# Kernel optimization log

Hardware: AMD Instinct MI355X
Metric: run time of the kernel (lower is better)

The kernel has to match this reference:

```python
import jax, jax.numpy as jnp
import numpy as np

B, F_IN, HID, H, S = 256, 1024, 1024, 16, 128
TEMP = float((HID // H) ** 0.5)  # 8.0


def setup_inputs() -> dict:
    key = jax.random.key(0)
    ks = jax.random.split(key, 7)
    return {
        "x": jax.random.normal(ks[0], (B, F_IN, S), dtype=jnp.float32),
        "Wq": jax.random.normal(ks[1], (HID, F_IN), dtype=jnp.float32) * (1.0 / np.sqrt(F_IN)),
        "bq": jax.random.normal(ks[2], (HID,), dtype=jnp.float32) * 0.01,
        "Wk": jax.random.normal(ks[3], (HID, F_IN), dtype=jnp.float32) * (1.0 / np.sqrt(F_IN)),
        "bk": jax.random.normal(ks[4], (HID,), dtype=jnp.float32) * 0.01,
        "Wo": jax.random.normal(ks[5], (S,), dtype=jnp.float32) * (1.0 / np.sqrt(S)),
        "bo": jax.random.normal(ks[6], (1,), dtype=jnp.float32) * 0.01,
    }


def _to_heads(t):
    # (B, F, S) -> (B, H, S, F//H), matching reshape(B,H,F/H,S).permute(0,1,3,2)
    b, f, s = t.shape
    return t.reshape(b, H, f // H, s).transpose(0, 1, 3, 2)


def reference(x, Wq, bq, Wk, bk, Wo, bo):
    # 1x1 Conv1d == per-position linear over channel dim
    q = jnp.einsum('bis,hi->bhs', x, Wq) + bq[None, :, None]
    k = jnp.einsum('bis,hi->bhs', x, Wk) + bk[None, :, None]
    qh = _to_heads(q)          # (B,H,S,HID/H)
    kh = _to_heads(k)          # (B,H,S,HID/H)
    vh = _to_heads(x)          # (B,H,S,F_IN/H)  -- v is the raw input, unprojected
    scores = jnp.einsum('bhsd,bhtd->bhst', qh, kh) / TEMP
    attn = jax.nn.softmax(scores, axis=-1)
    out = jnp.einsum('bhst,bhtd->bhsd', attn, vh)   # (B,H,S,F_IN/H)
    # _reshape_from_batches: (B,H,S,dv) -> (B, F_IN, S)
    out = out.transpose(0, 1, 3, 2).reshape(x.shape[0], F_IN, S)
    # map_o: Linear(num_users, 1) over last axis, then squeeze
    score = jnp.einsum('bfs,s->bf', out, Wo) + bo[0]
    return score
```

## Files before the change

### kernel.cpp

```cpp
#include <hip/hip_runtime.h>

#define F 1024
#define S 128
#define H 16
#define D 64
#define CK 64
#define NCHUNK 16

typedef short bf16x8 __attribute__((ext_vector_type(8)));
typedef float f32x4  __attribute__((ext_vector_type(4)));

#define XS_UNITS ((size_t)128 * NCHUNK * 2048)
#define WB_UNITS ((size_t)8 * NCHUNK * 2048)
#define WS_NEED ((XS_UNITS + WB_UNITS) * 16)

#define MAIN_LDS_BYTES (8192 * 16 + 8 * 128 * 4 + 128 * 4)

__device__ __forceinline__ unsigned short f2bf(float f) {
    unsigned u = __float_as_uint(f);
    u += 0x7fffu + ((u >> 16) & 1u);
    return (unsigned short)(u >> 16);
}

__device__ __forceinline__ float bf2f(unsigned short h) {
    return __uint_as_float((unsigned)h << 16);
}

__device__ __forceinline__ uint4 pack8(const float* f) {
    uint4 u;
    u.x = (unsigned)f2bf(f[0]) | ((unsigned)f2bf(f[1]) << 16);
    u.y = (unsigned)f2bf(f[2]) | ((unsigned)f2bf(f[3]) << 16);
    u.z = (unsigned)f2bf(f[4]) | ((unsigned)f2bf(f[5]) << 16);
    u.w = (unsigned)f2bf(f[6]) | ((unsigned)f2bf(f[7]) << 16);
    return u;
}

typedef __attribute__((address_space(1))) const unsigned int as1_u32;
typedef __attribute__((address_space(3))) unsigned int as3_u32;

__device__ __forceinline__ void async_cp16(const uint4* g, uint4* l) {
    __builtin_amdgcn_global_load_lds((as1_u32*)g, (as3_u32*)l, 16, 0, 0);
}

__device__ __forceinline__ void bar()   { __builtin_amdgcn_s_barrier(); }
__device__ __forceinline__ void sb0()   { __builtin_amdgcn_sched_barrier(0); }
__device__ __forceinline__ void lgkm0() { asm volatile("s_waitcnt lgkmcnt(0)"); }

template<int N> __device__ __forceinline__ void vmw() {
    asm volatile("s_waitcnt vmcnt(%0)" :: "n"(N));
}

__global__ void prep(const float* __restrict__ x,
                     const float* __restrict__ Wq,
                     const float* __restrict__ Wk,
                     uint4* __restrict__ xs,
                     uint4* __restrict__ wb)
{
    __shared__ float4 t4[64 * 33];
    const int tid = threadIdx.x;
    const int blk = blockIdx.x;
    if (blk < 4096) {
        const int b = blk >> 4, ch = blk & 15;
        const float4* src = (const float4*)(x + ((size_t)b * F + ch * CK) * S);
        float4 v[8];
#pragma unroll
        for (int j = 0; j < 8; ++j) v[j] = src[tid + j * 256];
#pragma unroll
        for (int j = 0; j < 8; ++j) {
            const int e4 = tid + j * 256;
            t4[(e4 >> 5) * 33 + (e4 & 31)] = v[j];
        }
        __syncthreads();
        const float* tile = (const float*)t4;
        uint4* dst = xs + ((size_t)(b >> 1) * NCHUNK + ch) * 2048 + (b & 1) * 128;
#pragma unroll
        for (int j = 0; j < 4; ++j) {
            const int u  = tid + j * 256;
            const int kc = u >> 7;
            const int s  = u & 127;
            float f[8];
#pragma unroll
            for (int jj = 0; jj < 8; ++jj) f[jj] = tile[(kc * 8 + jj) * 132 + s];
            dst[kc * 256 + s] = pack8(f);
        }
    } else {
        const int blk2 = blk - 4096;
        const int h = blk2 >> 4, ch = blk2 & 15;
        uint4* dst = wb + ((size_t)(h >> 1) * NCHUNK + ch) * 2048 + (h & 1) * 128;
#pragma unroll
        for (int j = 0; j < 4; ++j) {
            const int u  = tid + j * 256;
            const int kc = u >> 7;
            const int m  = u & 127;
            const float* srcp = (m < 64)
                ? (Wq + (size_t)(h * D + m) * F + ch * CK + kc * 8)
                : (Wk + (size_t)(h * D + m - 64) * F + ch * CK + kc * 8);
            float f[8];
            float4 a = ((const float4*)srcp)[0];
            float4 c = ((const float4*)srcp)[1];
            f[0] = a.x; f[1] = a.y; f[2] = a.z; f[3] = a.w;
            f[4] = c.x; f[5] = c.y; f[6] = c.z; f[7] = c.w;
            dst[kc * 256 + m] = pack8(f);
        }
    }
}

__device__ __forceinline__ void read4(const uint4* mat, int base, bf16x8 (&r)[4]) {
    r[0] = *(const bf16x8*)&mat[base];
    r[1] = *(const bf16x8*)&mat[base + 16];
    r[2] = *(const bf16x8*)&mat[base + 32];
    r[3] = *(const bf16x8*)&mat[base + 48];
}

template<int RB>
__device__ __forceinline__ void mfma16(f32x4 (&acc)[8][4], const bf16x8 (&af)[4], const bf16x8 (&br)[4]) {
#pragma unroll
    for (int mt = 0; mt < 4; ++mt)
#pragma unroll
        for (int nt = 0; nt < 4; ++nt)
            acc[RB + mt][nt] = __builtin_amdgcn_mfma_f32_16x16x32_bf16(af[mt], br[nt], acc[RB + mt][nt], 0, 0, 0);
}

template<int HALF>
__device__ __forceinline__ void stage_half(uint4* mat, const uint4* wbase, const uint4* xbase,
                                           int tgt, int wv, int lane) {
    const int bufb = (tgt & 1) * 4096;
    const uint4* g;
    int l;
    if constexpr (HALF == 0)      { g = wbase + (size_t)tgt * 2048;        l = bufb;        }
    else if constexpr (HALF == 1) { g = xbase + (size_t)tgt * 2048;        l = bufb + 2048; }
    else if constexpr (HALF == 2) { g = wbase + (size_t)tgt * 2048 + 1024; l = bufb + 1024; }
    else                          { g = xbase + (size_t)tgt * 2048 + 1024; l = bufb + 3072; }
    async_cp16(g + wv * 128 + lane,      &mat[l + wv * 128]);
    async_cp16(g + wv * 128 + 64 + lane, &mat[l + wv * 128 + 64]);
}

template<int CUR, bool I1, bool I2, int W1, int W2, bool DW2>
__device__ __forceinline__ void ktile(uint4* mat, const uint4* wbase, const uint4* xbase,
                                      int t, int wv, int lane, int wm, int wn, int q, int l15,
                                      f32x4 (&acc)[8][4])
{
    bf16x8 af[4], br[4];
    const int abase = CUR * 4096 + wm * 128 + l15;
    const int bbase = CUR * 4096 + 2048 + wn * 64 + l15;
    const int kq = q * 256;
    read4(mat, abase + kq, af);
    read4(mat, bbase + kq, br);
    if constexpr (I1) stage_half<2>(mat, wbase, xbase, t + 1, wv, lane);
    bar(); lgkm0(); sb0();
    __builtin_amdgcn_s_setprio(1); mfma16<0>(acc, af, br); __builtin_amdgcn_s_setprio(0);
    bar(); sb0();
    read4(mat, abase + kq + 64, af);
    if constexpr (I1) stage_half<3>(mat, wbase, xbase, t + 1, wv, lane);
    bar(); lgkm0(); sb0();
    __builtin_amdgcn_s_setprio(1); mfma16<4>(acc, af, br); __builtin_amdgcn_s_setprio(0);
    vmw<W1>(); bar(); sb0();
    read4(mat, abase + kq + 1024, af);
    read4(mat, bbase + kq + 1024, br);
    if constexpr (I2) stage_half<0>(mat, wbase, xbase, t + 2, wv, lane);
    bar(); lgkm0(); sb0();
    __builtin_amdgcn_s_setprio(1); mfma16<0>(acc, af, br); __builtin_amdgcn_s_setprio(0);
    bar(); sb0();
    read4(mat, abase + kq + 1024 + 64, af);
    if constexpr (I2) stage_half<1>(mat, wbase, xbase, t + 2, wv, lane);
    bar(); lgkm0(); sb0();
    __builtin_amdgcn_s_setprio(1); mfma16<4>(acc, af, br); __builtin_amdgcn_s_setprio(0);
    if constexpr (DW2) { vmw<W2>(); bar(); sb0(); }
}

__launch_bounds__(512, 2)
__global__ void attn_main(const float* __restrict__ x,
                          const uint4* __restrict__ xs,
                          const uint4* __restrict__ wb,
                          const float* __restrict__ bq,
                          const float* __restrict__ bk,
                          const float* __restrict__ Wo,
                          const float* __restrict__ bo,
                          float* __restrict__ out)
{
    (void)x;
    extern __shared__ char smraw[];
    uint4* mat   = (uint4*)smraw;
    float* wpart = (float*)(smraw + 8192 * 16);
    float* wfin  = wpart + 8 * 128;

    const int tid  = threadIdx.x;
    const int lane = tid & 63;
    const int wv   = tid >> 6;
    const int l15  = lane & 15;
    const int q    = lane >> 4;
    const int wm   = wv >> 2;
    const int wn   = wv & 3;

    const int g    = blockIdx.x;
    const int xcd  = g & 7;
    const int slot = g >> 3;
    const int bg   = xcd * 16 + (slot & 15);
    const int hg   = slot >> 4;

    const uint4* wbase = wb + (size_t)hg * NCHUNK * 2048;
    const uint4* xbase = xs + (size_t)bg * NCHUNK * 2048;

    f32x4 acc[8][4];
#pragma unroll
    for (int mi = 0; mi < 8; ++mi)
#pragma unroll
        for (int ni = 0; ni < 4; ++ni) acc[mi][ni] = (f32x4){0.f, 0.f, 0.f, 0.f};

    stage_half<0>(mat, wbase, xbase, 0, wv, lane);
    stage_half<1>(mat, wbase, xbase, 0, wv, lane);
    stage_half<2>(mat, wbase, xbase, 0, wv, lane);
    stage_half<3>(mat, wbase, xbase, 0, wv, lane);
    stage_half<0>(mat, wbase, xbase, 1, wv, lane);
    stage_half<1>(mat, wbase, xbase, 1, wv, lane);
    vmw<8>();
    bar(); sb0();

#pragma unroll 1
    for (int i = 0; i < 7; ++i) {
        ktile<0, true, true, 8, 8, true>(mat, wbase, xbase, 2 * i,     wv, lane, wm, wn, q, l15, acc);
        ktile<1, true, true, 8, 8, true>(mat, wbase, xbase, 2 * i + 1, wv, lane, wm, wn, q, l15, acc);
    }
    ktile<0, true,  false, 8, 4, true >(mat, wbase, xbase, 14, wv, lane, wm, wn, q, l15, acc);
    ktile<1, false, false, 0, 0, false>(mat, wbase, xbase, 15, wv, lane, wm, wn, q, l15, acc);

    __syncthreads();

    {
        unsigned short* m16 = (unsigned short*)mat;
        const int hglob = hg * 2 + wm;
#pragma unroll
        for (int rt = 0; rt < 8; ++rt) {
            const int mh0   = rt * 16 + q * 4;
            const int d0    = mh0 & 63;
            const int kbase = (mh0 < 64) ? 0 : 1024;
            float bias4[4];
#pragma unroll
            for (int rr = 0; rr < 4; ++rr)
                bias4[rr] = (mh0 < 64) ? bq[hglob * D + d0 + rr] : bk[hglob * D + d0 + rr];
#pragma unroll
            for (int ct = 0; ct < 4; ++ct) {
                const int col = wn * 64 + ct * 16 + l15;
                const int bj  = col >> 7;
                const int s   = col & 127;
                const int c   = wm * 2 + bj;
                unsigned long long pv = 0;
#pragma unroll
                for (int rr = 0; rr < 4; ++rr)
                    pv |= (unsigned long long)f2bf(acc[rt][ct][rr] + bias4[rr]) << (16 * rr);
                const int unit = c * 2048 + kbase + s * 8 + ((d0 >> 3) ^ (s & 7));
                *(unsigned long long*)&m16[unit * 8 + (d0 & 7)] = pv;
            }
        }
    }
    __syncthreads();

    for (int c = 0; c < 4; ++c) {
        const int qb = c * 2048;
        const int kb = c * 2048 + 1024;
        const int bglob = bg * 2 + (c & 1);
        const int hglob = hg * 2 + (c >> 1);

        f32x4 p[8];
#pragma unroll
        for (int nt = 0; nt < 8; ++nt) p[nt] = (f32x4){0.f, 0.f, 0.f, 0.f};
#pragma unroll
        for (int ks = 0; ks < 2; ++ks) {
            const int kcq  = ks * 4 + q;
            const int arow = wv * 16 + l15;
            bf16x8 a2 = *(const bf16x8*)&mat[qb + arow * 8 + (kcq ^ (arow & 7))];
            bf16x8 b2[8];
#pragma unroll
            for (int nt = 0; nt < 8; ++nt) {
                const int trow = nt * 16 + l15;
                b2[nt] = *(const bf16x8*)&mat[kb + trow * 8 + (kcq ^ (trow & 7))];
            }
#pragma unroll
            for (int nt = 0; nt < 8; ++nt)
                p[nt] = __builtin_amdgcn_mfma_f32_16x16x32_bf16(a2, b2[nt], p[nt], 0, 0, 0);
        }

        const int dd = tid >> 3, part = tid & 7;
        const unsigned short* xp = (const unsigned short*)(xbase + (size_t)hglob * 2048);
        const int hw0 = ((dd >> 3) * 256 + (bglob & 1) * 128) * 8 + (dd & 7);
        unsigned short xr[16];
#pragma unroll
        for (int jj = 0; jj < 16; ++jj) xr[jj] = xp[hw0 + (part * 16 + jj) * 8];

        float pw[8];
#pragma unroll
        for (int nt = 0; nt < 8; ++nt) pw[nt] = 0.f;
#pragma unroll
        for (int rr = 0; rr < 4; ++rr) {
            const int srow = wv * 16 + q * 4 + rr;
            float mx = p[0][rr];
#pragma unroll
            for (int nt = 1; nt < 8; ++nt) mx = fmaxf(mx, p[nt][rr]);
#pragma unroll
            for (int off = 1; off < 16; off <<= 1) mx = fmaxf(mx, __shfl_xor(mx, off));
            float e[8];
            float l = 0.f;
#pragma unroll
            for (int nt = 0; nt < 8; ++nt) {
                e[nt] = __expf((p[nt][rr] - mx) * 0.125f);
                l += e[nt];
            }
#pragma unroll
            for (int off = 1; off < 16; off <<= 1) l += __shfl_xor(l, off);
            const float cw = Wo[srow] / l;
#pragma unroll
            for (int nt = 0; nt < 8; ++nt) pw[nt] = fmaf(cw, e[nt], pw[nt]);
        }
#pragma unroll
        for (int nt = 0; nt < 8; ++nt) {
            pw[nt] += __shfl_xor(pw[nt], 16);
            pw[nt] += __shfl_xor(pw[nt], 32);
        }
        if (q == 0) {
#pragma unroll
            for (int nt = 0; nt < 8; ++nt) wpart[wv * 128 + nt * 16 + l15] = pw[nt];
        }
        __syncthreads();
        if (tid < 128) {
            float sum = 0.f;
#pragma unroll
            for (int w = 0; w < 8; ++w) sum += wpart[w * 128 + tid];
            wfin[tid] = sum;
        }
        __syncthreads();
        {
            float a5 = 0.f;
#pragma unroll
            for (int jj = 0; jj < 16; ++jj)
                a5 = fmaf(wfin[part * 16 + jj], bf2f(xr[jj]), a5);
            a5 += __shfl_xor(a5, 1);
            a5 += __shfl_xor(a5, 2);
            a5 += __shfl_xor(a5, 4);
            if (part == 0) out[(size_t)bglob * F + hglob * D + dd] = a5 + bo[0];
        }
        __syncthreads();
    }
}

struct SmemT {
    uint4 mat[2048];
    float wpart[4][S];
    float wfin[S];
};

__launch_bounds__(256, 4)
__global__ void attn_fallback(const float* __restrict__ x,
                              const float* __restrict__ Wq,
                              const float* __restrict__ bq,
                              const float* __restrict__ Wk,
                              const float* __restrict__ bk,
                              const float* __restrict__ Wo,
                              const float* __restrict__ bo,
                              float* __restrict__ out)
{
    __shared__ SmemT sm;
    const int tid  = threadIdx.x;
    const int lane = tid & 63;
    const int wv   = tid >> 6;
    const int l15  = lane & 15;
    const int q    = lane >> 4;

    const int g    = blockIdx.x;
    const int xcd  = g & 7;
    const int slot = g >> 3;
    const int hg   = slot >> 7;
    const int r0   = slot & 127;
    const int b    = xcd * 32 + (r0 >> 2);
    const int h    = hg * 4 + (r0 & 3);

    const float* xb  = x  + (size_t)b * (F * S);
    const float* wqh = Wq + (size_t)h * D * F;
    const float* wkh = Wk + (size_t)h * D * F;

    const int m0 = (wv & 1) * 64;
    const int n0 = (wv >> 1) * 64;

    f32x4 acc[4][4];
#pragma unroll
    for (int mt = 0; mt < 4; ++mt)
#pragma unroll
        for (int nt = 0; nt < 4; ++nt) acc[mt][nt] = (f32x4){0.f, 0.f, 0.f, 0.f};

    const int mq  = tid >> 2;
    const int kq  = tid & 3;
    const int s0x = (tid & 63) * 2;
    const int iq  = tid >> 6;

    for (int ch = 0; ch < NCHUNK; ++ch) {
        const int c0 = ch * CK;
        __syncthreads();
        {
            const int key = mq & 7;
            float f[16];
            const float4* srcq = (const float4*)(wqh + (size_t)mq * F + (c0 + kq * 16));
#pragma unroll
            for (int j = 0; j < 4; ++j) {
                float4 v = srcq[j];
                f[4*j] = v.x; f[4*j+1] = v.y; f[4*j+2] = v.z; f[4*j+3] = v.w;
            }
            sm.mat[mq * 8 + ((kq * 2    ) ^ key)] = pack8(f);
            sm.mat[mq * 8 + ((kq * 2 + 1) ^ key)] = pack8(f + 8);
            const float4* srck = (const float4*)(wkh + (size_t)mq * F + (c0 + kq * 16));
#pragma unroll
            for (int j = 0; j < 4; ++j) {
                float4 v = srck[j];
                f[4*j] = v.x; f[4*j+1] = v.y; f[4*j+2] = v.z; f[4*j+3] = v.w;
            }
            sm.mat[(64 + mq) * 8 + ((kq * 2    ) ^ key)] = pack8(f);
            sm.mat[(64 + mq) * 8 + ((kq * 2 + 1) ^ key)] = pack8(f + 8);
        }
        {
            const float* src = xb + (size_t)(c0 + iq * 16) * S + s0x;
            float fa[8], fb[8];
#pragma unroll
            for (int grp = 0; grp < 2; ++grp) {
#pragma unroll
                for (int j = 0; j < 8; ++j) {
                    float2 v = *(const float2*)(src + (size_t)(grp * 8 + j) * S);
                    fa[j] = v.x; fb[j] = v.y;
                }
                const int kc = iq * 2 + grp;
                sm.mat[1024 + (s0x    ) * 8 + (kc ^ ((s0x    ) & 7))] = pack8(fa);
                sm.mat[1024 + (s0x + 1) * 8 + (kc ^ ((s0x + 1) & 7))] = pack8(fb);
            }
        }
        __syncthreads();
#pragma unroll
        for (int ks = 0; ks < 2; ++ks) {
            bf16x8 af[4], br[4];
#pragma unroll
            for (int mt = 0; mt < 4; ++mt) {
                const int row = m0 + mt * 16 + l15;
                af[mt] = *(const bf16x8*)&sm.mat[row * 8 + ((ks * 4 + q) ^ (row & 7))];
            }
#pragma unroll
            for (int nt = 0; nt < 4; ++nt) {
                const int row = n0 + nt * 16 + l15;
                br[nt] = *(const bf16x8*)&sm.mat[1024 + row * 8 + ((ks * 4 + q) ^ (row & 7))];
            }
#pragma unroll
            for (int mt = 0; mt < 4; ++mt)
#pragma unroll
                for (int nt = 0; nt < 4; ++nt)
                    acc[mt][nt] = __builtin_amdgcn_mfma_f32_16x16x32_bf16(
                        af[mt], br[nt], acc[mt][nt], 0, 0, 0);
        }
    }

    __syncthreads();
    {
        unsigned short* m16 = (unsigned short*)sm.mat;
#pragma unroll
        for (int mt = 0; mt < 4; ++mt) {
#pragma unroll
            for (int rr = 0; rr < 4; ++rr) {
                const int m = m0 + mt * 16 + q * 4 + rr;
                const int d = m & 63;
                const float bias = (m < 64) ? bq[h * D + d] : bk[h * D + d];
                const int base = (m < 64) ? 0 : 8192;
#pragma unroll
                for (int nt = 0; nt < 4; ++nt) {
                    const int s = n0 + nt * 16 + l15;
                    const float v = acc[mt][nt][rr] + bias;
                    const int unit = s * 8 + (((d >> 3)) ^ (s & 7));
                    m16[base + unit * 8 + (d & 7)] = f2bf(v);
                }
            }
        }
    }
    __syncthreads();

    f32x4 p[2][8];
#pragma unroll
    for (int mt = 0; mt < 2; ++mt)
#pragma unroll
        for (int nt = 0; nt < 8; ++nt) p[mt][nt] = (f32x4){0.f, 0.f, 0.f, 0.f};

#pragma unroll
    for (int ks = 0; ks < 2; ++ks) {
        bf16x8 a2[2], b2[8];
#pragma unroll
        for (int mt = 0; mt < 2; ++mt) {
            const int row = wv * 32 + mt * 16 + l15;
            a2[mt] = *(const bf16x8*)&sm.mat[row * 8 + ((ks * 4 + q) ^ (row & 7))];
        }
#pragma unroll
        for (int nt = 0; nt < 8; ++nt) {
            const int row = nt * 16 + l15;
            b2[nt] = *(const bf16x8*)&sm.mat[1024 + row * 8 + ((ks * 4 + q) ^ (row & 7))];
        }
#pragma unroll
        for (int mt = 0; mt < 2; ++mt)
#pragma unroll
            for (int nt = 0; nt < 8; ++nt)
                p[mt][nt] = __builtin_amdgcn_mfma_f32_16x16x32_bf16(a2[mt], b2[nt], p[mt][nt], 0, 0, 0);
    }

    float pw[8];
#pragma unroll
    for (int nt = 0; nt < 8; ++nt) pw[nt] = 0.f;

#pragma unroll
    for (int mt = 0; mt < 2; ++mt) {
#pragma unroll
        for (int rr = 0; rr < 4; ++rr) {
            const int srow = wv * 32 + mt * 16 + q * 4 + rr;
            float mx = p[mt][0][rr];
#pragma unroll
            for (int nt = 1; nt < 8; ++nt) mx = fmaxf(mx, p[mt][nt][rr]);
#pragma unroll
            for (int off = 1; off < 16; off <<= 1) mx = fmaxf(mx, __shfl_xor(mx, off));
            float e[8];
            float l = 0.f;
#pragma unroll
            for (int nt = 0; nt < 8; ++nt) {
                e[nt] = __expf((p[mt][nt][rr] - mx) * 0.125f);
                l += e[nt];
            }
#pragma unroll
            for (int off = 1; off < 16; off <<= 1) l += __shfl_xor(l, off);
            const float c = Wo[srow] / l;
#pragma unroll
            for (int nt = 0; nt < 8; ++nt) pw[nt] = fmaf(c, e[nt], pw[nt]);
        }
    }
#pragma unroll
    for (int nt = 0; nt < 8; ++nt) {
        pw[nt] += __shfl_xor(pw[nt], 16);
        pw[nt] += __shfl_xor(pw[nt], 32);
    }
    if (q == 0) {
#pragma unroll
        for (int nt = 0; nt < 8; ++nt) sm.wpart[wv][nt * 16 + l15] = pw[nt];
    }
    __syncthreads();
    if (tid < S)
        sm.wfin[tid] = sm.wpart[0][tid] + sm.wpart[1][tid] + sm.wpart[2][tid] + sm.wpart[3][tid];
    __syncthreads();

    {
        const int dd   = tid >> 2;
        const int part = tid & 3;
        const float* xv = xb + (size_t)(h * D + dd) * S + part * 32;
        float a5 = 0.f;
#pragma unroll 8
        for (int t = 0; t < 32; ++t) a5 = fmaf(sm.wfin[part * 32 + t], xv[t], a5);
        a5 += __shfl_xor(a5, 1);
        a5 += __shfl_xor(a5, 2);
        if (part == 0) out[(size_t)b * F + h * D + dd] = a5 + bo[0];
    }
}

extern "C" void kernel_launch(void* const* d_in, const int* in_sizes, int n_in,
                              void* d_out, int out_size, void* d_ws, size_t ws_size,
                              hipStream_t stream) {
    const float* x  = (const float*)d_in[0];
    const float* Wq = (const float*)d_in[1];
    const float* bq = (const float*)d_in[2];
    const float* Wk = (const float*)d_in[3];
    const float* bk = (const float*)d_in[4];
    const float* Wo = (const float*)d_in[5];
    const float* bo = (const float*)d_in[6];
    float* out = (float*)d_out;

    if (ws_size >= WS_NEED) {
        uint4* xsp = (uint4*)d_ws;
        uint4* wbp = (uint4*)((char*)d_ws + XS_UNITS * 16);
        static bool attr_done = false;
        if (!attr_done) {
            (void)hipFuncSetAttribute(reinterpret_cast<const void*>(attn_main),
                                      hipFuncAttributeMaxDynamicSharedMemorySize, MAIN_LDS_BYTES);
            attr_done = true;
        }
        prep<<<dim3(4096 + 256), dim3(256), 0, stream>>>(x, Wq, Wk, xsp, wbp);
        attn_main<<<dim3(1024), dim3(512), MAIN_LDS_BYTES, stream>>>(x, xsp, wbp, bq, bk, Wo, bo, out);
    } else {
        attn_fallback<<<dim3(256 * H), dim3(256), 0, stream>>>(x, Wq, bq, Wk, bk, Wo, bo, out);
    }
}
```

Baseline: 378.0 us.

## Process four attention combos concurrently, drop softmax max pass, coarsen prep blocks

```diff
diff --git a/kernel.cpp b/kernel.cpp
--- a/kernel.cpp
+++ b/kernel.cpp
@@ -20,10 +20,6 @@
     unsigned u = __float_as_uint(f);
     u += 0x7fffu + ((u >> 16) & 1u);
     return (unsigned short)(u >> 16);
-}
-
-__device__ __forceinline__ float bf2f(unsigned short h) {
-    return __uint_as_float((unsigned)h << 16);
 }
 
 __device__ __forceinline__ uint4 pack8(const float* f) {
@@ -59,48 +55,57 @@
     __shared__ float4 t4[64 * 33];
     const int tid = threadIdx.x;
     const int blk = blockIdx.x;
-    if (blk < 4096) {
-        const int b = blk >> 4, ch = blk & 15;
-        const float4* src = (const float4*)(x + ((size_t)b * F + ch * CK) * S);
-        float4 v[8];
-#pragma unroll
-        for (int j = 0; j < 8; ++j) v[j] = src[tid + j * 256];
-#pragma unroll
-        for (int j = 0; j < 8; ++j) {
-            const int e4 = tid + j * 256;
-            t4[(e4 >> 5) * 33 + (e4 & 31)] = v[j];
-        }
-        __syncthreads();
-        const float* tile = (const float*)t4;
-        uint4* dst = xs + ((size_t)(b >> 1) * NCHUNK + ch) * 2048 + (b & 1) * 128;
-#pragma unroll
-        for (int j = 0; j < 4; ++j) {
-            const int u  = tid + j * 256;
-            const int kc = u >> 7;
-            const int s  = u & 127;
-            float f[8];
-#pragma unroll
-            for (int jj = 0; jj < 8; ++jj) f[jj] = tile[(kc * 8 + jj) * 132 + s];
-            dst[kc * 256 + s] = pack8(f);
+    if (blk < 1024) {
+        const int b = blk >> 2;
+#pragma unroll 1
+        for (int cc = 0; cc < 4; ++cc) {
+            const int ch = (blk & 3) * 4 + cc;
+            const float4* src = (const float4*)(x + ((size_t)b * F + ch * CK) * S);
+            float4 v[8];
+#pragma unroll
+            for (int j = 0; j < 8; ++j) v[j] = src[tid + j * 256];
+            __syncthreads();
+#pragma unroll
+            for (int j = 0; j < 8; ++j) {
+                const int e4 = tid + j * 256;
+                t4[(e4 >> 5) * 33 + (e4 & 31)] = v[j];
+            }
+            __syncthreads();
+            const float* tile = (const float*)t4;
+            uint4* dst = xs + ((size_t)(b >> 1) * NCHUNK + ch) * 2048 + (b & 1) * 128;
+#pragma unroll
+            for (int j = 0; j < 4; ++j) {
+                const int u  = tid + j * 256;
+                const int kc = u >> 7;
+                const int s  = u & 127;
+                float f[8];
+#pragma unroll
+                for (int jj = 0; jj < 8; ++jj) f[jj] = tile[(kc * 8 + jj) * 132 + s];
+                dst[kc * 256 + s] = pack8(f);
+            }
         }
     } else {
-        const int blk2 = blk - 4096;
-        const int h = blk2 >> 4, ch = blk2 & 15;
-        uint4* dst = wb + ((size_t)(h >> 1) * NCHUNK + ch) * 2048 + (h & 1) * 128;
-#pragma unroll
-        for (int j = 0; j < 4; ++j) {
-            const int u  = tid + j * 256;
-            const int kc = u >> 7;
-            const int m  = u & 127;
-            const float* srcp = (m < 64)
-                ? (Wq + (size_t)(h * D + m) * F + ch * CK + kc * 8)
-                : (Wk + (size_t)(h * D + m - 64) * F + ch * CK + kc * 8);
-            float f[8];
-            float4 a = ((const float4*)srcp)[0];
-            float4 c = ((const float4*)srcp)[1];
-            f[0] = a.x; f[1] = a.y; f[2] = a.z; f[3] = a.w;
-            f[4] = c.x; f[5] = c.y; f[6] = c.z; f[7] = c.w;
-            dst[kc * 256 + m] = pack8(f);
+        const int blk2 = blk - 1024;
+        const int h = blk2 >> 2;
+#pragma unroll 1
+        for (int cc = 0; cc < 4; ++cc) {
+            const int ch = (blk2 & 3) * 4 + cc;
+            uint4* dst = wb + ((size_t)(h >> 1) * NCHUNK + ch) * 2048 + (h & 1) * 128;
+#pragma unroll
+            for (int j = 0; j < 4; ++j) {
+                const int u  = tid + j * 256;
+                const int kc = u >> 7;
+                const int m  = u & 127;
+                const float* srcp = (m < 64)
+                    ? (Wq + (size_t)(h * D + m) * F + ch * CK + kc * 8)
+                    : (Wk + (size_t)(h * D + m - 64) * F + ch * CK + kc * 8);
+                float f[8];
+                float4 a = ((const float4*)srcp)[0];
+                float4 c = ((const float4*)srcp)[1];
+                f[0] = a.x; f[1] = a.y; f[2] = a.z; f[3] = a.w;
+                f[4] = c.x; f[5] = c.y; f[6] = c.z; f[7] = c.w;
+                dst[kc * 256 + m] = pack8(f);
+            }
         }
     }
 }
@@ -178,11 +183,9 @@
                           const float* __restrict__ bo,
                           float* __restrict__ out)
 {
-    (void)x;
     extern __shared__ char smraw[];
     uint4* mat   = (uint4*)smraw;
     float* wpart = (float*)(smraw + 8192 * 16);
-    float* wfin  = wpart + 8 * 128;
 
     const int tid  = threadIdx.x;
     const int lane = tid & 63;
@@ -255,54 +258,52 @@
     }
     __syncthreads();
 
-    for (int c = 0; c < 4; ++c) {
-        const int qb = c * 2048;
-        const int kb = c * 2048 + 1024;
-        const int bglob = bg * 2 + (c & 1);
-        const int hglob = hg * 2 + (c >> 1);
-
-        f32x4 p[8];
-#pragma unroll
-        for (int nt = 0; nt < 8; ++nt) p[nt] = (f32x4){0.f, 0.f, 0.f, 0.f};
-#pragma unroll
-        for (int ks = 0; ks < 2; ++ks) {
-            const int kcq  = ks * 4 + q;
-            const int arow = wv * 16 + l15;
-            bf16x8 a2 = *(const bf16x8*)&mat[qb + arow * 8 + (kcq ^ (arow & 7))];
-            bf16x8 b2[8];
-#pragma unroll
-            for (int nt = 0; nt < 8; ++nt) {
-                const int trow = nt * 16 + l15;
-                b2[nt] = *(const bf16x8*)&mat[kb + trow * 8 + (kcq ^ (trow & 7))];
-            }
+    const int ce   = ((wv >> 2) << 1) | ((wv >> 1) & 1);
+    const int half = wv & 1;
+    const int qb = ce * 2048;
+    const int kb = ce * 2048 + 1024;
+    const int bglob = bg * 2 + (ce & 1);
+    const int hglob = hg * 2 + (ce >> 1);
+
+    f32x4 p[4][8];
+#pragma unroll
+    for (int mt = 0; mt < 4; ++mt)
+#pragma unroll
+        for (int nt = 0; nt < 8; ++nt) p[mt][nt] = (f32x4){0.f, 0.f, 0.f, 0.f};
+#pragma unroll
+    for (int ks = 0; ks < 2; ++ks) {
+        const int kcq = ks * 4 + q;
+        bf16x8 a2[4], b2[8];
+#pragma unroll
+        for (int mt = 0; mt < 4; ++mt) {
+            const int row = half * 64 + mt * 16 + l15;
+            a2[mt] = *(const bf16x8*)&mat[qb + row * 8 + (kcq ^ (row & 7))];
+        }
+#pragma unroll
+        for (int nt = 0; nt < 8; ++nt) {
+            const int trow = nt * 16 + l15;
+            b2[nt] = *(const bf16x8*)&mat[kb + trow * 8 + (kcq ^ (trow & 7))];
+        }
+#pragma unroll
+        for (int mt = 0; mt < 4; ++mt)
 #pragma unroll
             for (int nt = 0; nt < 8; ++nt)
-                p[nt] = __builtin_amdgcn_mfma_f32_16x16x32_bf16(a2, b2[nt], p[nt], 0, 0, 0);
-        }
-
-        const int dd = tid >> 3, part = tid & 7;
-        const unsigned short* xp = (const unsigned short*)(xbase + (size_t)hglob * 2048);
-        const int hw0 = ((dd >> 3) * 256 + (bglob & 1) * 128) * 8 + (dd & 7);
-        unsigned short xr[16];
-#pragma unroll
-        for (int jj = 0; jj < 16; ++jj) xr[jj] = xp[hw0 + (part * 16 + jj) * 8];
-
-        float pw[8];
-#pragma unroll
-        for (int nt = 0; nt < 8; ++nt) pw[nt] = 0.f;
+                p[mt][nt] = __builtin_amdgcn_mfma_f32_16x16x32_bf16(a2[mt], b2[nt], p[mt][nt], 0, 0, 0);
+    }
+
+    float pw[8];
+#pragma unroll
+    for (int nt = 0; nt < 8; ++nt) pw[nt] = 0.f;
+#pragma unroll
+    for (int mt = 0; mt < 4; ++mt) {
 #pragma unroll
         for (int rr = 0; rr < 4; ++rr) {
-            const int srow = wv * 16 + q * 4 + rr;
-            float mx = p[0][rr];
-#pragma unroll
-            for (int nt = 1; nt < 8; ++nt) mx = fmaxf(mx, p[nt][rr]);
-#pragma unroll
-            for (int off = 1; off < 16; off <<= 1) mx = fmaxf(mx, __shfl_xor(mx, off));
+            const int srow = half * 64 + mt * 16 + q * 4 + rr;
             float e[8];
             float l = 0.f;
 #pragma unroll
             for (int nt = 0; nt < 8; ++nt) {
-                e[nt] = __expf((p[nt][rr] - mx) * 0.125f);
+                e[nt] = __expf(fminf(p[mt][nt][rr] * 0.125f, 80.f));
                 l += e[nt];
             }
 #pragma unroll
@@ -311,34 +312,38 @@
 #pragma unroll
             for (int nt = 0; nt < 8; ++nt) pw[nt] = fmaf(cw, e[nt], pw[nt]);
         }
-#pragma unroll
-        for (int nt = 0; nt < 8; ++nt) {
-            pw[nt] += __shfl_xor(pw[nt], 16);
-            pw[nt] += __shfl_xor(pw[nt], 32);
-        }
-        if (q == 0) {
-#pragma unroll
-            for (int nt = 0; nt < 8; ++nt) wpart[wv * 128 + nt * 16 + l15] = pw[nt];
-        }
-        __syncthreads();
-        if (tid < 128) {
-            float sum = 0.f;
-#pragma unroll
-            for (int w = 0; w < 8; ++w) sum += wpart[w * 128 + tid];
-            wfin[tid] = sum;
-        }
-        __syncthreads();
-        {
-            float a5 = 0.f;
-#pragma unroll
-            for (int jj = 0; jj < 16; ++jj)
-                a5 = fmaf(wfin[part * 16 + jj], bf2f(xr[jj]), a5);
-            a5 += __shfl_xor(a5, 1);
-            a5 += __shfl_xor(a5, 2);
-            a5 += __shfl_xor(a5, 4);
-            if (part == 0) out[(size_t)bglob * F + hglob * D + dd] = a5 + bo[0];
-        }
-        __syncthreads();
+    }
+#pragma unroll
+    for (int nt = 0; nt < 8; ++nt) {
+        pw[nt] += __shfl_xor(pw[nt], 16);
+        pw[nt] += __shfl_xor(pw[nt], 32);
+    }
+    if (q == 0) {
+#pragma unroll
+        for (int nt = 0; nt < 8; ++nt) wpart[wv * 128 + nt * 16 + l15] = pw[nt];
+    }
+    __syncthreads();
+
+    {
+        const int local = half * 64 + lane;
+        const int dd    = local >> 1;
+        const int part  = local & 1;
+        const float* w0 = wpart + 2 * ce * 128;
+        const float* w1 = wpart + (2 * ce + 1) * 128;
+        const float4* xv = (const float4*)(x + (size_t)bglob * (F * S)
+                                             + (size_t)(hglob * D + dd) * S + part * 64);
+        float a5 = 0.f;
+#pragma unroll
+        for (int j = 0; j < 16; ++j) {
+            float4 vv = xv[j];
+            const int t = part * 64 + j * 4;
+            a5 = fmaf(w0[t + 0] + w1[t + 0], vv.x, a5);
+            a5 = fmaf(w0[t + 1] + w1[t + 1], vv.y, a5);
+            a5 = fmaf(w0[t + 2] + w1[t + 2], vv.z, a5);
+            a5 = fmaf(w0[t + 3] + w1[t + 3], vv.w, a5);
+        }
+        a5 += __shfl_xor(a5, 1);
+        if (part == 0) out[(size_t)bglob * F + hglob * D + dd] = a5 + bo[0];
     }
 }
 
@@ -577,7 +582,7 @@
                                       hipFuncAttributeMaxDynamicSharedMemorySize, MAIN_LDS_BYTES);
             attr_done = true;
         }
-        prep<<<dim3(4096 + 256), dim3(256), 0, stream>>>(x, Wq, Wk, xsp, wbp);
+        prep<<<dim3(1024 + 64), dim3(256), 0, stream>>>(x, Wq, Wk, xsp, wbp);
         attn_main<<<dim3(1024), dim3(512), MAIN_LDS_BYTES, stream>>>(x, xsp, wbp, bq, bk, Wo, bo, out);
     } else {
         attn_fallback<<<dim3(256 * H), dim3(256), 0, stream>>>(x, Wq, bq, Wk, bk, Wo, bo, out);
```

Measured after the change: 397.4 us. 1.05x slower.
